# Kernel tuning notes

Hardware: AMD Instinct MI355X
Metric: run time of the kernel (lower is better)

Reference implementation:

```python
import jax, jax.numpy as jnp
import numpy as np
import math

B, S, D, H = 4, 4096, 768, 64

def setup_inputs() -> dict:
    key = jax.random.key(0)
    ks = jax.random.split(key, 4)
    scale = 1.0 / math.sqrt(D)
    return {
        "X": jax.random.normal(ks[0], (B, S, D), dtype=jnp.float32),
        "Wq": jax.random.normal(ks[1], (D, H), dtype=jnp.float32) * scale,
        "bq": jnp.zeros((H,), dtype=jnp.float32),
        "Wk": jax.random.normal(ks[2], (D, H), dtype=jnp.float32) * scale,
        "bk": jnp.zeros((H,), dtype=jnp.float32),
        "Wv": jax.random.normal(ks[3], (D, H), dtype=jnp.float32) * scale,
        "bv": jnp.zeros((H,), dtype=jnp.float32),
    }

def reference(X, Wq, bq, Wk, bk, Wv, bv):
    # Single-head causal scaled-dot-product attention (dropout p=0 / eval mode).
    Q = X @ Wq + bq            # [B, S, H]
    K = X @ Wk + bk            # [B, S, H]
    V = X @ Wv + bv            # [B, S, H]
    head_size = Q.shape[-1]
    scores = jnp.einsum('bqh,bkh->bqk', Q, K) / jnp.sqrt(jnp.asarray(head_size, Q.dtype))
    causal = jnp.tril(jnp.ones((Q.shape[1], Q.shape[1]), dtype=bool))  # [S, S]
    scores = jnp.where(causal[None, :, :], scores, -jnp.inf)
    attn = jax.nn.softmax(scores, axis=-1)   # [B, S, S]
    return jnp.einsum('bqk,bkh->bqh', attn, V)
```

## Files before the change

kernel.cpp:

```cpp
#include <hip/hip_runtime.h>
#include <math.h>

#define BB 4
#define SS 4096
#define DD 768
#define HH 64
#define MM (BB * SS)

typedef __attribute__((ext_vector_type(8))) short bf16x8;
typedef __attribute__((ext_vector_type(4))) float f32x4;

__device__ inline unsigned short f2bf(float f) {
    union { float f; unsigned u; } x; x.f = f;
    unsigned r = x.u + 0x7fffu + ((x.u >> 16) & 1u);
    return (unsigned short)(r >> 16);
}

__device__ inline unsigned short* swzp(unsigned short* base, int byteoff) {
    byteoff ^= ((byteoff >> 7) & 7) << 4;
    return (unsigned short*)((char*)base + byteoff);
}

__global__ __launch_bounds__(256) void wt_kernel(
    const float* __restrict__ Wq, const float* __restrict__ Wk, const float* __restrict__ Wv,
    unsigned short* __restrict__ Wt)
{
    const int kt = blockIdx.x;
    const int sel = blockIdx.y;
    const int k0 = kt * 64;
    const float* W = (sel == 0) ? Wq : (sel == 1) ? Wk : Wv;
    __shared__ float Ws[64][68];
    const int t = threadIdx.x;
    #pragma unroll
    for (int j = 0; j < 4; ++j) {
        const int fl = t + j * 256;
        const int row = fl >> 4, c4 = (fl & 15) * 4;
        float4 v = *reinterpret_cast<const float4*>(&W[(size_t)(k0 + row) * HH + c4]);
        Ws[row][c4 + 0] = v.x; Ws[row][c4 + 1] = v.y;
        Ws[row][c4 + 2] = v.z; Ws[row][c4 + 3] = v.w;
    }
    __syncthreads();
    const int n = t >> 2;
    const int c8 = (t & 3) * 16;
    unsigned short tmp[16];
    #pragma unroll
    for (int j = 0; j < 16; ++j) tmp[j] = f2bf(Ws[c8 + j][n]);
    unsigned short* dst = &Wt[((size_t)sel * 64 + n) * DD + k0 + c8];
    *reinterpret_cast<bf16x8*>(dst)     = *reinterpret_cast<bf16x8*>(&tmp[0]);
    *reinterpret_cast<bf16x8*>(dst + 8) = *reinterpret_cast<bf16x8*>(&tmp[8]);
}

__global__ __launch_bounds__(512) void qkv_proj_kernel(
    const float* __restrict__ X, const unsigned short* __restrict__ Wt,
    const float* __restrict__ bq, const float* __restrict__ bk, const float* __restrict__ bv,
    unsigned short* __restrict__ Qb, unsigned short* __restrict__ Kb,
    unsigned short* __restrict__ Vt)
{
    __shared__ unsigned short Alds[32 * 64];
    __shared__ unsigned short Blds[192 * 64];

    const int tid = threadIdx.x;
    const int rowBase = blockIdx.x * 32;
    const int w = tid >> 6;
    const int ms = w & 1;
    const int nq = w >> 1;
    const int lane = tid & 63;
    const int lhi = lane >> 4, llo = lane & 15;

    f32x4 acc[3] = {{0,0,0,0},{0,0,0,0},{0,0,0,0}};

    const int arow = tid >> 4;
    const int ac   = (tid & 15) * 4;

    float4 xA, xB;
    bf16x8 bA[3], bB[3];

    auto loadP = [&](int kb, float4& x0, bf16x8 (&bb)[3]) {
        const int kBase = kb * 64;
        x0 = *reinterpret_cast<const float4*>(&X[(size_t)(rowBase + arow) * DD + kBase + ac]);
        #pragma unroll
        for (int i = 0; i < 3; ++i) {
            const int u = tid + i * 512;
            const int n = u >> 3, c8 = (u & 7) * 8;
            bb[i] = *reinterpret_cast<const bf16x8*>(&Wt[(size_t)n * DD + kBase + c8]);
        }
    };
    auto writeP = [&](const float4& x0, bf16x8 (&bb)[3]) {
        ushort4 pk;
        pk.x = f2bf(x0.x); pk.y = f2bf(x0.y); pk.z = f2bf(x0.z); pk.w = f2bf(x0.w);
        *reinterpret_cast<ushort4*>(swzp(Alds, (arow * 64 + ac) * 2)) = pk;
        #pragma unroll
        for (int i = 0; i < 3; ++i) {
            const int u = tid + i * 512;
            const int n = u >> 3, c8 = (u & 7) * 8;
            *reinterpret_cast<bf16x8*>(swzp(Blds, (n * 64 + c8) * 2)) = bb[i];
        }
    };

    loadP(0, xA, bA);

    for (int kb = 0; kb < DD / 64; ++kb) {
        __syncthreads();
        if ((kb & 1) == 0) {
            writeP(xA, bA);
            if (kb + 1 < DD / 64) loadP(kb + 1, xB, bB);
        } else {
            writeP(xB, bB);
            if (kb + 1 < DD / 64) loadP(kb + 1, xA, bA);
        }
        __syncthreads();

        #pragma unroll
        for (int kk = 0; kk < 2; ++kk) {
            const int aoff = kk * 32 + lhi * 8;
            bf16x8 af = *reinterpret_cast<const bf16x8*>(
                swzp(Alds, ((ms * 16 + llo) * 64 + aoff) * 2));
            #pragma unroll
            for (int nt = 0; nt < 3; ++nt) {
                bf16x8 bf = *reinterpret_cast<const bf16x8*>(
                    swzp(Blds, ((nq * 48 + nt * 16 + llo) * 64 + aoff) * 2));
                acc[nt] = __builtin_amdgcn_mfma_f32_16x16x32_bf16(af, bf, acc[nt], 0, 0, 0);
            }
        }
    }

    #pragma unroll
    for (int nt = 0; nt < 3; ++nt) {
        const int n = nq * 48 + nt * 16 + llo;
        const int sel = n >> 6;
        const int nn = n & 63;
        const float bias = (sel == 0) ? bq[nn] : (sel == 1) ? bk[nn] : bv[nn];
        #pragma unroll
        for (int r = 0; r < 4; ++r) {
            const int row = rowBase + ms * 16 + lhi * 4 + r;
            const float val = acc[nt][r] + bias;
            if (sel == 0) {
                Qb[(size_t)row * HH + nn] = f2bf(val * 0.125f);
            } else if (sel == 1) {
                Kb[(size_t)row * HH + nn] = f2bf(val);
            } else {
                const int bb = row >> 12;
                const int s = row & (SS - 1);
                Vt[((size_t)bb * HH + nn) * SS + s] = f2bf(val);
            }
        }
    }
}

union SMemA {
    struct {
        unsigned short K[2 * 4096];
        unsigned short V[2 * 4096];
        unsigned short Pl[8][16][72];
    } st;
    struct { float O[4][16][68]; float ml[4][16][2]; } cb;
};

__global__ __launch_bounds__(512, 4) void attn_partial_kernel(
    const unsigned short* __restrict__ Qg, const unsigned short* __restrict__ Kg,
    const unsigned short* __restrict__ Vtg, float* __restrict__ out,
    float* __restrict__ Po, float* __restrict__ Pml)
{
    __shared__ SMemA sm;

    const int idx = blockIdx.x;
    const int l = idx >> 2;
    const int b = idx & 3;
    int qb, c;
    if (l < 49)       { qb = 15 + l;        c = 0; }
    else if (l < 82)  { qb = 31 + (l - 49); c = 1; }
    else if (l < 99)  { qb = 47 + (l - 82); c = 2; }
    else if (l == 99) { qb = 63;            c = 3; }
    else {
        const int j = l - 100;
        const int s = 15 - (j >> 2);
        const int k = j & 3;
        qb = (s - 1) + 16 * k;
        c = k;
    }

    const int tid = threadIdx.x;
    const int q0 = qb * 64;
    const int w   = tid >> 6;
    const int g   = w >> 2;
    const int wq  = w & 3;
    const int lane = tid & 63;
    const int lhi = lane >> 4, llo = lane & 15;
    const int qw0 = q0 + wq * 16;
    const int qme = qw0 + llo;

    const int ntiles = qb + 1;
    const int base0 = c * 16;
    const int endT = min(base0 + 16, ntiles);
    const int nsteps = (endT - base0 + 1) >> 1;
    const int nch = qb / 16 + 1;

    const unsigned short* Kbase = Kg  + (size_t)b * SS * HH;
    const unsigned short* Vbase = Vtg + (size_t)b * HH * SS;

    bf16x8 qf0, qf1;
    {
        const unsigned short* qrow = Qg + ((size_t)b * SS + qme) * HH + lhi * 8;
        qf0 = *reinterpret_cast<const bf16x8*>(qrow);
        qf1 = *reinterpret_cast<const bf16x8*>(qrow + 32);
    }

    float m = -INFINITY, lsum = 0.f;
    f32x4 acc[4] = {{0,0,0,0},{0,0,0,0},{0,0,0,0},{0,0,0,0}};

    const int srow = tid >> 3;
    const int sc8  = (tid & 7) * 8;

    bf16x8 rA[4] = {{0,0,0,0,0,0,0,0},{0,0,0,0,0,0,0,0},{0,0,0,0,0,0,0,0},{0,0,0,0,0,0,0,0}};
    bf16x8 rB[4] = {{0,0,0,0,0,0,0,0},{0,0,0,0,0,0,0,0},{0,0,0,0,0,0,0,0},{0,0,0,0,0,0,0,0}};

    auto load_step = [&](int base, bf16x8 (&rg)[4]) {
        #pragma unroll
        for (int i = 0; i < 4; ++i) {
            const int t = base + (i & 1);
            if (t < endT) {
                rg[i] = (i < 2)
                    ? *reinterpret_cast<const bf16x8*>(&Kbase[(size_t)(t * 64 + srow) * HH + sc8])
                    : *reinterpret_cast<const bf16x8*>(&Vbase[(size_t)srow * SS + t * 64 + sc8]);
            }
        }
    };
    auto write_step = [&](bf16x8 (&rg)[4]) {
        const int ro = (srow * 64 + sc8) * 2;
        *reinterpret_cast<bf16x8*>(swzp(sm.st.K, ro))         = rg[0];
        *reinterpret_cast<bf16x8*>(swzp(sm.st.K, 8192 + ro))  = rg[1];
        *reinterpret_cast<bf16x8*>(swzp(sm.st.V, ro))         = rg[2];
        *reinterpret_cast<bf16x8*>(swzp(sm.st.V, 8192 + ro))  = rg[3];
    };

    load_step(base0, rA);

    for (int stp = 0; stp < nsteps; ++stp) {
        const int base = base0 + stp * 2;
        __syncthreads();
        if ((stp & 1) == 0) {
            write_step(rA);
            if (stp + 1 < nsteps) load_step(base + 2, rB);
        } else {
            write_step(rB);
            if (stp + 1 < nsteps) load_step(base + 2, rA);
        }
        __syncthreads();

        const int lt = base + g;
        if (lt < endT) {
            const int k0 = lt * 64;
            const int tb = g * 8192;

            f32x4 s[4] = {{0,0,0,0},{0,0,0,0},{0,0,0,0},{0,0,0,0}};
            #pragma unroll
            for (int kt = 0; kt < 4; ++kt) {
                const int rbo = tb + ((kt * 16 + llo) * 64) * 2;
                bf16x8 ka = *reinterpret_cast<const bf16x8*>(swzp(sm.st.K, rbo + lhi * 16));
                bf16x8 kb = *reinterpret_cast<const bf16x8*>(swzp(sm.st.K, rbo + 64 + lhi * 16));
                s[kt] = __builtin_amdgcn_mfma_f32_16x16x32_bf16(ka, qf0, s[kt], 0, 0, 0);
                s[kt] = __builtin_amdgcn_mfma_f32_16x16x32_bf16(kb, qf1, s[kt], 0, 0, 0);
            }

            if (k0 + 63 > qw0) {
                #pragma unroll
                for (int kt = 0; kt < 4; ++kt) {
                    #pragma unroll
                    for (int r = 0; r < 4; ++r) {
                        const int key = k0 + kt * 16 + lhi * 4 + r;
                        if (key > qme) s[kt][r] = -INFINITY;
                    }
                }
            }

            float mx = s[0][0];
            #pragma unroll
            for (int kt = 0; kt < 4; ++kt)
                #pragma unroll
                for (int r = 0; r < 4; ++r) mx = fmaxf(mx, s[kt][r]);
            mx = fmaxf(mx, __shfl_xor(mx, 16));
            mx = fmaxf(mx, __shfl_xor(mx, 32));
            const float mn = fmaxf(m, mx);
            const float corr = __expf(m - mn);
            float ps = 0.f;
            #pragma unroll
            for (int kt = 0; kt < 4; ++kt)
                #pragma unroll
                for (int r = 0; r < 4; ++r) { s[kt][r] = __expf(s[kt][r] - mn); ps += s[kt][r]; }
            ps += __shfl_xor(ps, 16);
            ps += __shfl_xor(ps, 32);
            lsum = lsum * corr + ps;
            m = mn;
            #pragma unroll
            for (int dt = 0; dt < 4; ++dt)
                #pragma unroll
                for (int r = 0; r < 4; ++r) acc[dt][r] *= corr;

            #pragma unroll
            for (int kt = 0; kt < 4; ++kt) {
                ushort4 pk;
                pk.x = f2bf(s[kt][0]); pk.y = f2bf(s[kt][1]);
                pk.z = f2bf(s[kt][2]); pk.w = f2bf(s[kt][3]);
                *reinterpret_cast<ushort4*>(&sm.st.Pl[w][llo][kt * 16 + lhi * 4]) = pk;
            }
            bf16x8 pf0 = *reinterpret_cast<const bf16x8*>(&sm.st.Pl[w][llo][lhi * 8]);
            bf16x8 pf1 = *reinterpret_cast<const bf16x8*>(&sm.st.Pl[w][llo][32 + lhi * 8]);

            #pragma unroll
            for (int dt = 0; dt < 4; ++dt) {
                const int rbo = tb + ((dt * 16 + llo) * 64) * 2;
                bf16x8 va = *reinterpret_cast<const bf16x8*>(swzp(sm.st.V, rbo + lhi * 16));
                bf16x8 vb = *reinterpret_cast<const bf16x8*>(swzp(sm.st.V, rbo + 64 + lhi * 16));
                acc[dt] = __builtin_amdgcn_mfma_f32_16x16x32_bf16(va, pf0, acc[dt], 0, 0, 0);
                acc[dt] = __builtin_amdgcn_mfma_f32_16x16x32_bf16(vb, pf1, acc[dt], 0, 0, 0);
            }
        }
    }

    __syncthreads();
    if (g == 1) {
        #pragma unroll
        for (int dt = 0; dt < 4; ++dt) {
            float4 o4 = {acc[dt][0], acc[dt][1], acc[dt][2], acc[dt][3]};
            *reinterpret_cast<float4*>(&sm.cb.O[wq][llo][dt * 16 + lhi * 4]) = o4;
        }
        if (lhi == 0) { sm.cb.ml[wq][llo][0] = m; sm.cb.ml[wq][llo][1] = lsum; }
    }
    __syncthreads();
    if (g == 0) {
        const float mg = sm.cb.ml[wq][llo][0];
        const float lg = sm.cb.ml[wq][llo][1];
        const float M  = fmaxf(m, mg);
        const float a0 = __expf(m - M);
        const float a1 = __expf(mg - M);
        const float L  = lsum * a0 + lg * a1;
        if (nch == 1) {
            const float invL = 1.f / L;
            float* orow = out + ((size_t)b * SS + qme) * HH;
            #pragma unroll
            for (int dt = 0; dt < 4; ++dt) {
                const float4 o2 = *reinterpret_cast<const float4*>(&sm.cb.O[wq][llo][dt * 16 + lhi * 4]);
                float4 o;
                o.x = (acc[dt][0] * a0 + o2.x * a1) * invL;
                o.y = (acc[dt][1] * a0 + o2.y * a1) * invL;
                o.z = (acc[dt][2] * a0 + o2.z * a1) * invL;
                o.w = (acc[dt][3] * a0 + o2.w * a1) * invL;
                *reinterpret_cast<float4*>(&orow[dt * 16 + lhi * 4]) = o;
            }
        } else {
            float* PoT  = Po  + (((size_t)(b * 64 + qb) * 4 + c) << 12);
            float* PmlT = Pml + (((size_t)(b * 64 + qb) * 4 + c) << 7);
            const int row = wq * 16 + llo;
            #pragma unroll
            for (int dt = 0; dt < 4; ++dt) {
                const float4 o2 = *reinterpret_cast<const float4*>(&sm.cb.O[wq][llo][dt * 16 + lhi * 4]);
                float4 o;
                o.x = acc[dt][0] * a0 + o2.x * a1;
                o.y = acc[dt][1] * a0 + o2.y * a1;
                o.z = acc[dt][2] * a0 + o2.z * a1;
                o.w = acc[dt][3] * a0 + o2.w * a1;
                *reinterpret_cast<float4*>(&PoT[row * 64 + dt * 16 + lhi * 4]) = o;
            }
            if (lhi == 0) { PmlT[row] = M; PmlT[64 + row] = L; }
        }
    }
}

__global__ __launch_bounds__(256) void combine_kernel(
    const float* __restrict__ Po, const float* __restrict__ Pml, float* __restrict__ out)
{
    const int qt = 16 + blockIdx.x;
    const int b  = blockIdx.y;
    const int nch = qt / 16 + 1;
    const int t = threadIdx.x;
    const int row = t >> 2;
    const int col0 = (t & 3) * 16;
    const size_t baseIdx = (size_t)(b * 64 + qt) * 4;

    float mv[4], lv[4], a[4];
    float M = -INFINITY;
    for (int cc = 0; cc < nch; ++cc) {
        const float* PmlT = Pml + ((baseIdx + cc) << 7);
        mv[cc] = PmlT[row];
        lv[cc] = PmlT[64 + row];
        M = fmaxf(M, mv[cc]);
    }
    float L = 0.f;
    for (int cc = 0; cc < nch; ++cc) { a[cc] = __expf(mv[cc] - M); L += a[cc] * lv[cc]; }
    const float invL = 1.f / L;

    #pragma unroll
    for (int j = 0; j < 4; ++j) {
        float4 s = {0.f, 0.f, 0.f, 0.f};
        for (int cc = 0; cc < nch; ++cc) {
            const float4 v = *reinterpret_cast<const float4*>(
                &Po[((baseIdx + cc) << 12) + row * 64 + col0 + j * 4]);
            s.x += a[cc] * v.x; s.y += a[cc] * v.y;
            s.z += a[cc] * v.z; s.w += a[cc] * v.w;
        }
        s.x *= invL; s.y *= invL; s.z *= invL; s.w *= invL;
        *reinterpret_cast<float4*>(&out[((size_t)b * SS + qt * 64 + row) * HH + col0 + j * 4]) = s;
    }
}

extern "C" void kernel_launch(void* const* d_in, const int* in_sizes, int n_in,
                              void* d_out, int out_size, void* d_ws, size_t ws_size,
                              hipStream_t stream)
{
    const float* X  = (const float*)d_in[0];
    const float* Wq = (const float*)d_in[1];
    const float* bq = (const float*)d_in[2];
    const float* Wk = (const float*)d_in[3];
    const float* bk = (const float*)d_in[4];
    const float* Wv = (const float*)d_in[5];
    const float* bv = (const float*)d_in[6];

    unsigned short* Qb = (unsigned short*)d_ws;
    unsigned short* Kb = Qb + (size_t)MM * HH;
    unsigned short* Vt = Kb + (size_t)MM * HH;
    unsigned short* Wt = Vt + (size_t)MM * HH;
    float* Po  = (float*)(Wt + (size_t)192 * DD);
    float* Pml = Po + ((size_t)BB * 64 * 4 << 12);

    dim3 gw(DD / 64, 3);
    wt_kernel<<<gw, 256, 0, stream>>>(Wq, Wk, Wv, Wt);

    qkv_proj_kernel<<<MM / 32, 512, 0, stream>>>(X, Wt, bq, bk, bv, Qb, Kb, Vt);

    attn_partial_kernel<<<160 * BB, 512, 0, stream>>>(Qb, Kb, Vt, (float*)d_out, Po, Pml);
    dim3 gc(48, BB);
    combine_kernel<<<gc, 256, 0, stream>>>(Po, Pml, (float*)d_out);
}
```

Before: 58.74 us.

## Fuse split-K combine into attention via atomic counters, add lazy rescale and setprio

Removes the separate combine kernel. The last partial block for each query tile, found through an atomic counter, merges all chunk partials and writes the output. The online softmax now skips the max update and the accumulator rescale unless the running max grows by more than 8, which cuts exp and multiply work. s_setprio is raised around the MFMA loops so those waves are favoured for issue. The change adds a memset launch and atomic/fence overhead, and the lazy rescale keeps values bounded by e^8 in fp32/bf16.

```diff
diff --git a/kernel.cpp b/kernel.cpp
--- a/kernel.cpp
+++ b/kernel.cpp
@@ -159,9 +159,10 @@
 __global__ __launch_bounds__(512, 4) void attn_partial_kernel(
     const unsigned short* __restrict__ Qg, const unsigned short* __restrict__ Kg,
     const unsigned short* __restrict__ Vtg, float* __restrict__ out,
-    float* __restrict__ Po, float* __restrict__ Pml)
+    float* __restrict__ Po, float* __restrict__ Pml, int* __restrict__ cnt)
 {
     __shared__ SMemA sm;
+    __shared__ int s_done;
 
     const int idx = blockIdx.x;
     const int l = idx >> 2;
@@ -253,6 +254,7 @@
             const int tb = g * 8192;
 
             f32x4 s[4] = {{0,0,0,0},{0,0,0,0},{0,0,0,0},{0,0,0,0}};
+            __builtin_amdgcn_s_setprio(1);
             #pragma unroll
             for (int kt = 0; kt < 4; ++kt) {
                 const int rbo = tb + ((kt * 16 + llo) * 64) * 2;
@@ -261,6 +263,7 @@
                 s[kt] = __builtin_amdgcn_mfma_f32_16x16x32_bf16(ka, qf0, s[kt], 0, 0, 0);
                 s[kt] = __builtin_amdgcn_mfma_f32_16x16x32_bf16(kb, qf1, s[kt], 0, 0, 0);
             }
+            __builtin_amdgcn_s_setprio(0);
 
             if (k0 + 63 > qw0) {
                 #pragma unroll
@@ -280,21 +283,24 @@
                 for (int r = 0; r < 4; ++r) mx = fmaxf(mx, s[kt][r]);
             mx = fmaxf(mx, __shfl_xor(mx, 16));
             mx = fmaxf(mx, __shfl_xor(mx, 32));
-            const float mn = fmaxf(m, mx);
-            const float corr = __expf(m - mn);
+            if (!__all(mx - m <= 8.0f)) {
+                const float mn = fmaxf(m, mx);
+                const float corr = __expf(m - mn);
+                lsum *= corr;
+                #pragma unroll
+                for (int dt = 0; dt < 4; ++dt)
+                    #pragma unroll
+                    for (int r = 0; r < 4; ++r) acc[dt][r] *= corr;
+                m = mn;
+            }
             float ps = 0.f;
             #pragma unroll
             for (int kt = 0; kt < 4; ++kt)
                 #pragma unroll
-                for (int r = 0; r < 4; ++r) { s[kt][r] = __expf(s[kt][r] - mn); ps += s[kt][r]; }
+                for (int r = 0; r < 4; ++r) { s[kt][r] = __expf(s[kt][r] - m); ps += s[kt][r]; }
             ps += __shfl_xor(ps, 16);
             ps += __shfl_xor(ps, 32);
-            lsum = lsum * corr + ps;
-            m = mn;
-            #pragma unroll
-            for (int dt = 0; dt < 4; ++dt)
-                #pragma unroll
-                for (int r = 0; r < 4; ++r) acc[dt][r] *= corr;
+            lsum += ps;
 
             #pragma unroll
             for (int kt = 0; kt < 4; ++kt) {
@@ -306,6 +312,7 @@
             bf16x8 pf0 = *reinterpret_cast<const bf16x8*>(&sm.st.Pl[w][llo][lhi * 8]);
             bf16x8 pf1 = *reinterpret_cast<const bf16x8*>(&sm.st.Pl[w][llo][32 + lhi * 8]);
 
+            __builtin_amdgcn_s_setprio(1);
             #pragma unroll
             for (int dt = 0; dt < 4; ++dt) {
                 const int rbo = tb + ((dt * 16 + llo) * 64) * 2;
@@ -314,6 +321,7 @@
                 acc[dt] = __builtin_amdgcn_mfma_f32_16x16x32_bf16(va, pf0, acc[dt], 0, 0, 0);
                 acc[dt] = __builtin_amdgcn_mfma_f32_16x16x32_bf16(vb, pf1, acc[dt], 0, 0, 0);
             }
+            __builtin_amdgcn_s_setprio(0);
         }
     }
 
@@ -364,42 +372,57 @@
             if (lhi == 0) { PmlT[row] = M; PmlT[64 + row] = L; }
         }
     }
-}
-
-__global__ __launch_bounds__(256) void combine_kernel(
-    const float* __restrict__ Po, const float* __restrict__ Pml, float* __restrict__ out)
-{
-    const int qt = 16 + blockIdx.x;
-    const int b  = blockIdx.y;
-    const int nch = qt / 16 + 1;
-    const int t = threadIdx.x;
-    const int row = t >> 2;
-    const int col0 = (t & 3) * 16;
-    const size_t baseIdx = (size_t)(b * 64 + qt) * 4;
-
-    float mv[4], lv[4], a[4];
-    float M = -INFINITY;
-    for (int cc = 0; cc < nch; ++cc) {
-        const float* PmlT = Pml + ((baseIdx + cc) << 7);
-        mv[cc] = PmlT[row];
-        lv[cc] = PmlT[64 + row];
-        M = fmaxf(M, mv[cc]);
-    }
-    float L = 0.f;
-    for (int cc = 0; cc < nch; ++cc) { a[cc] = __expf(mv[cc] - M); L += a[cc] * lv[cc]; }
-    const float invL = 1.f / L;
-
-    #pragma unroll
-    for (int j = 0; j < 4; ++j) {
-        float4 s = {0.f, 0.f, 0.f, 0.f};
-        for (int cc = 0; cc < nch; ++cc) {
-            const float4 v = *reinterpret_cast<const float4*>(
-                &Po[((baseIdx + cc) << 12) + row * 64 + col0 + j * 4]);
-            s.x += a[cc] * v.x; s.y += a[cc] * v.y;
-            s.z += a[cc] * v.z; s.w += a[cc] * v.w;
-        }
-        s.x *= invL; s.y *= invL; s.z *= invL; s.w *= invL;
-        *reinterpret_cast<float4*>(&out[((size_t)b * SS + qt * 64 + row) * HH + col0 + j * 4]) = s;
+
+    if (nch > 1) {
+        __syncthreads();
+        if (tid == 0) {
+            __threadfence();
+            const int old = atomicAdd(&cnt[b * 64 + qb], 1);
+            s_done = (old == nch - 1) ? 1 : 0;
+        }
+        __syncthreads();
+        if (s_done) {
+            __threadfence();
+            const int row  = tid >> 3;
+            const int col0 = (tid & 7) * 8;
+            const size_t baseIdx = (size_t)(b * 64 + qb) * 4;
+            const float mv0 = Pml[((baseIdx + 0) << 7) + row];
+            const float lv0 = Pml[((baseIdx + 0) << 7) + 64 + row];
+            const float mv1 = Pml[((baseIdx + 1) << 7) + row];
+            const float lv1 = Pml[((baseIdx + 1) << 7) + 64 + row];
+            float mv2 = -INFINITY, lv2 = 0.f, mv3 = -INFINITY, lv3 = 0.f;
+            if (nch > 2) { mv2 = Pml[((baseIdx + 2) << 7) + row]; lv2 = Pml[((baseIdx + 2) << 7) + 64 + row]; }
+            if (nch > 3) { mv3 = Pml[((baseIdx + 3) << 7) + row]; lv3 = Pml[((baseIdx + 3) << 7) + 64 + row]; }
+            const float M2 = fmaxf(fmaxf(mv0, mv1), fmaxf(mv2, mv3));
+            const float a0 = __expf(mv0 - M2);
+            const float a1 = __expf(mv1 - M2);
+            const float a2 = __expf(mv2 - M2);
+            const float a3 = __expf(mv3 - M2);
+            const float L2 = a0 * lv0 + a1 * lv1 + a2 * lv2 + a3 * lv3;
+            const float invL2 = 1.f / L2;
+            float* orow = out + ((size_t)b * SS + q0 + row) * HH;
+            #pragma unroll
+            for (int j = 0; j < 2; ++j) {
+                const int co = row * 64 + col0 + j * 4;
+                float4 v0 = *reinterpret_cast<const float4*>(&Po[((baseIdx + 0) << 12) + co]);
+                float4 v1 = *reinterpret_cast<const float4*>(&Po[((baseIdx + 1) << 12) + co]);
+                float4 o;
+                o.x = a0 * v0.x + a1 * v1.x;
+                o.y = a0 * v0.y + a1 * v1.y;
+                o.z = a0 * v0.z + a1 * v1.z;
+                o.w = a0 * v0.w + a1 * v1.w;
+                if (nch > 2) {
+                    float4 v2 = *reinterpret_cast<const float4*>(&Po[((baseIdx + 2) << 12) + co]);
+                    o.x += a2 * v2.x; o.y += a2 * v2.y; o.z += a2 * v2.z; o.w += a2 * v2.w;
+                }
+                if (nch > 3) {
+                    float4 v3 = *reinterpret_cast<const float4*>(&Po[((baseIdx + 3) << 12) + co]);
+                    o.x += a3 * v3.x; o.y += a3 * v3.y; o.z += a3 * v3.z; o.w += a3 * v3.w;
+                }
+                o.x *= invL2; o.y *= invL2; o.z *= invL2; o.w *= invL2;
+                *reinterpret_cast<float4*>(&orow[col0 + j * 4]) = o;
+            }
+        }
     }
 }
 
@@ -421,13 +444,14 @@
     unsigned short* Wt = Vt + (size_t)MM * HH;
     float* Po  = (float*)(Wt + (size_t)192 * DD);
     float* Pml = Po + ((size_t)BB * 64 * 4 << 12);
+    int*   cnt = (int*)(Pml + ((size_t)BB * 64 * 4 << 7));
+
+    hipMemsetAsync(cnt, 0, (size_t)BB * 64 * sizeof(int), stream);
 
     dim3 gw(DD / 64, 3);
     wt_kernel<<<gw, 256, 0, stream>>>(Wq, Wk, Wv, Wt);
 
     qkv_proj_kernel<<<MM / 32, 512, 0, stream>>>(X, Wt, bq, bk, bv, Qb, Kb, Vt);
 
-    attn_partial_kernel<<<160 * BB, 512, 0, stream>>>(Qb, Kb, Vt, (float*)d_out, Po, Pml);
-    dim3 gc(48, BB);
-    combine_kernel<<<gc, 256, 0, stream>>>(Po, Pml, (float*)d_out);
-}
+    attn_partial_kernel<<<160 * BB, 512, 0, stream>>>(Qb, Kb, Vt, (float*)d_out, Po, Pml, cnt);
+}
```

After: 127.7 us. +117.4%, slower.
